# Performance work log

Measured on AMD Instinct MI355X. Metric: run time of the kernel, lower is better.

Reference implementation:

```python
import jax, jax.numpy as jnp
import numpy as np

DIM = 96; HEADS = 3; HEAD_DIM = 32; INNER = HEADS * HEAD_DIM; MLP = 384
WS = 4; WV = WS ** 3; SHIFT = WS // 2  # displacement = window//2
SPATIAL = 64


def _rel_indices():
    c = np.stack(np.meshgrid(np.arange(WS), np.arange(WS), np.arange(WS), indexing='ij'), -1).reshape(-1, 3)
    return c[:, None] - c[None, :] + (WS - 1)  # [WV, WV, 3] in [0, 2*WS-2]

REL = _rel_indices()


def _make_mask():
    # standard Swin shifted-window mask: label contiguity regions, partition, -inf cross-region
    X = Y = Z = SPATIAL
    lab = np.zeros((X, Y, Z), np.int32); cnt = 0
    sl = (slice(0, -WS), slice(-WS, -SHIFT), slice(-SHIFT, None))
    for sx in sl:
        for sy in sl:
            for sz in sl:
                lab[sx, sy, sz] = cnt; cnt += 1
    n = X // WS
    lab = lab.reshape(n, WS, n, WS, n, WS).transpose(0, 2, 4, 1, 3, 5).reshape(-1, WV)
    m = np.where(lab[:, :, None] != lab[:, None, :], -1e9, 0.0).astype(np.float32)
    return jnp.asarray(m)  # [nW, WV, WV]

MASK = _make_mask()


def _ln(x, g, b):
    m = x.mean(-1, keepdims=True)
    v = ((x - m) ** 2).mean(-1, keepdims=True)
    return (x - m) * jax.lax.rsqrt(v + 1e-5) * g + b


def _window_attn(x, W_qkv, W_out, b_out, pos_tab):
    B, X, Y, Z, _ = x.shape
    x = jnp.roll(x, (-SHIFT, -SHIFT, -SHIFT), axis=(1, 2, 3))  # cyclic shift
    qkv = x @ W_qkv  # [B,X,Y,Z,3*INNER]
    nx, ny, nz = X // WS, Y // WS, Z // WS
    qkv = qkv.reshape(B, nx, WS, ny, WS, nz, WS, 3, HEADS, HEAD_DIM)
    qkv = qkv.transpose(7, 0, 8, 1, 3, 5, 2, 4, 6, 9).reshape(3, B, HEADS, nx * ny * nz, WV, HEAD_DIM)
    q, k, v = qkv[0], qkv[1], qkv[2]
    dots = jnp.einsum('bhwid,bhwjd->bhwij', q, k) * (HEAD_DIM ** -0.5)
    bias = pos_tab[REL[..., 0], REL[..., 1], REL[..., 2]]  # [WV,WV]
    dots = dots + bias + MASK[None, None]
    attn = jax.nn.softmax(dots, axis=-1)
    out = jnp.einsum('bhwij,bhwjd->bhwid', attn, v)
    out = out.reshape(B, HEADS, nx, ny, nz, WS, WS, WS, HEAD_DIM)
    out = out.transpose(0, 2, 5, 3, 6, 4, 7, 1, 8).reshape(B, X, Y, Z, INNER)
    out = out @ W_out + b_out
    return jnp.roll(out, (SHIFT, SHIFT, SHIFT), axis=(1, 2, 3))  # cyclic back-shift


def setup_inputs() -> dict:
    key = jax.random.key(0)
    ks = jax.random.split(key, 8)
    w = lambda k, shape, s=0.02: (jax.random.normal(k, shape, jnp.float32) * s)
    return {
        'x': jax.random.normal(ks[0], (1, SPATIAL, SPATIAL, SPATIAL, DIM), jnp.float32),
        'W_qkv': w(ks[1], (DIM, 3 * INNER)),
        'W_out': w(ks[2], (INNER, DIM)),
        'b_out': jnp.zeros((DIM,), jnp.float32),
        'pos_tab': w(ks[3], (2 * WS - 1, 2 * WS - 1, 2 * WS - 1), 1.0),
        'ln1_g': jnp.ones((DIM,), jnp.float32), 'ln1_b': jnp.zeros((DIM,), jnp.float32),
        'ln2_g': jnp.ones((DIM,), jnp.float32), 'ln2_b': jnp.zeros((DIM,), jnp.float32),
        'W1': w(ks[4], (DIM, MLP)), 'b1': jnp.zeros((MLP,), jnp.float32),
        'W2': w(ks[5], (MLP, DIM)), 'b2': jnp.zeros((DIM,), jnp.float32),
    }


def reference(x, W_qkv, W_out, b_out, pos_tab, ln1_g, ln1_b, ln2_g, ln2_b, W1, b1, W2, b2):
    # Residual(PreNorm(WindowAttention3D))
    x = x + _window_attn(_ln(x, ln1_g, ln1_b), W_qkv, W_out, b_out, pos_tab)
    # Residual(PreNorm(FeedForward3D)): Linear -> GELU -> Linear (dropout=0)
    h = _ln(x, ln2_g, ln2_b)
    h = jax.nn.gelu(h @ W1 + b1, approximate=False) @ W2 + b2
    return x + h
```

## Files before the change

### kernel.cpp

```cpp
#include <hip/hip_runtime.h>
#include <hip/hip_bf16.h>

typedef __attribute__((ext_vector_type(8))) short bf16x8;
typedef __attribute__((ext_vector_type(4))) short s16x4;
typedef __attribute__((ext_vector_type(4))) float f32x4;

#define NWIN 4096

__device__ __forceinline__ unsigned short f2bf(float f) {
    __hip_bfloat16 h = __float2bfloat16(f);
    unsigned short u;
    __builtin_memcpy(&u, &h, 2);
    return u;
}
__device__ __forceinline__ float bf2f(unsigned short u) {
    return __uint_as_float(((unsigned int)u) << 16);
}
__device__ __forceinline__ int region(int g) { return (g >= 60) + (g >= 62); }

__global__ void convert_weights(const float* __restrict__ Wqkv, const float* __restrict__ Wout,
                                const float* __restrict__ W1, const float* __restrict__ W2,
                                unsigned short* __restrict__ wq_t, unsigned short* __restrict__ wo_t,
                                unsigned short* __restrict__ w1_t, unsigned short* __restrict__ w2_t) {
    int idx = blockIdx.x * blockDim.x + threadIdx.x;
    if (idx < 27648) {
        int n = idx / 96, k = idx % 96;
        wq_t[idx] = f2bf(Wqkv[k * 288 + n]);
    } else if (idx < 27648 + 9216) {
        int i = idx - 27648; int n = i / 96, k = i % 96;
        wo_t[i] = f2bf(Wout[k * 96 + n]);
    } else if (idx < 27648 + 9216 + 36864) {
        int i = idx - 36864; int n = i / 96, k = i % 96;
        w1_t[i] = f2bf(W1[k * 384 + n]);
    } else if (idx < 110592) {
        int i = idx - 73728; int n = i / 384, k = i % 384;
        w2_t[i] = f2bf(W2[k * 96 + n]);
    }
}

__global__ __launch_bounds__(384, 4) void ln_qkv_attn_kernel(
    const float* __restrict__ x,
    const float* __restrict__ ln1_g, const float* __restrict__ ln1_b,
    const unsigned short* __restrict__ wq_t,
    const float* __restrict__ pos_tab,
    unsigned short* __restrict__ a_out)
{
    __shared__ __align__(16) unsigned short SH[22272];
    __shared__ __align__(16) float posl[344];
    unsigned short* q_s = SH;
    unsigned short* k_s = SH + 7680;
    unsigned short* vT  = SH + 15360;
    unsigned short* y_s = SH + 15360;
    unsigned short* P_s = SH;

    int win = blockIdx.x;
    int tid = threadIdx.x;
    int w = tid >> 6, lane = tid & 63, lr = lane & 15, kh = lane >> 4;
    int ix = win >> 8, iy = (win >> 4) & 15, iz = win & 15;

    if (tid < 343) posl[tid] = pos_tab[tid];

    {
        int grp = tid >> 4, gi = tid & 15;
        float gv[6], bv[6];
        #pragma unroll
        for (int j = 0; j < 6; ++j) { gv[j] = ln1_g[gi + 16 * j]; bv[j] = ln1_b[gi + 16 * j]; }
        #pragma unroll
        for (int p = 0; p < 3; ++p) {
            int t = grp + p * 24;
            if (t < 64) {
                int wx = t >> 4, wy = (t >> 2) & 3, wz = t & 3;
                int sx = (ix * 4 + wx + 2) & 63, sy = (iy * 4 + wy + 2) & 63, sz = (iz * 4 + wz + 2) & 63;
                const float* src = x + ((size_t)((sx * 64 + sy) * 64 + sz)) * 96;
                float v[6]; float s = 0.f, sq = 0.f;
                #pragma unroll
                for (int j = 0; j < 6; ++j) { v[j] = src[gi + 16 * j]; s += v[j]; sq += v[j] * v[j]; }
                #pragma unroll
                for (int m = 8; m >= 1; m >>= 1) { s += __shfl_xor(s, m, 16); sq += __shfl_xor(sq, m, 16); }
                float mean = s * (1.0f / 96.0f);
                float var = sq * (1.0f / 96.0f) - mean * mean;
                float rstd = rsqrtf(var + 1e-5f);
                #pragma unroll
                for (int j = 0; j < 6; ++j)
                    y_s[t * 104 + gi + 16 * j] = f2bf((v[j] - mean) * rstd * gv[j] + bv[j]);
            }
        }
    }
    __syncthreads();

    f32x4 acc3[4][3];
    {
        #pragma unroll
        for (int m = 0; m < 4; ++m)
            #pragma unroll
            for (int n = 0; n < 3; ++n) acc3[m][n] = (f32x4){0.f, 0.f, 0.f, 0.f};
        #pragma unroll
        for (int ks = 0; ks < 3; ++ks) {
            int k0 = ks * 32;
            bf16x8 a[4], bb[3];
            #pragma unroll
            for (int m = 0; m < 4; ++m)
                a[m] = *(const bf16x8*)&y_s[(m * 16 + lr) * 104 + k0 + kh * 8];
            #pragma unroll
            for (int n = 0; n < 3; ++n)
                bb[n] = *(const bf16x8*)(wq_t + (size_t)(w * 48 + n * 16 + lr) * 96 + k0 + kh * 8);
            #pragma unroll
            for (int m = 0; m < 4; ++m)
                #pragma unroll
                for (int n = 0; n < 3; ++n)
                    acc3[m][n] = __builtin_amdgcn_mfma_f32_16x16x32_bf16(a[m], bb[n], acc3[m][n], 0, 0, 0);
        }
    }
    __syncthreads();

    {
        const float scale = 0.17677669529663689f;
        #pragma unroll
        for (int n = 0; n < 3; ++n) {
            int base = w * 48 + n * 16;
            int qq = base / 96, cc0 = base % 96;
            int hh = cc0 >> 5, d0 = cc0 & 31;
            if (qq == 2) {
                #pragma unroll
                for (int m = 0; m < 4; ++m) {
                    s16x4 pv;
                    #pragma unroll
                    for (int r = 0; r < 4; ++r) pv[r] = (short)f2bf(acc3[m][n][r]);
                    *(s16x4*)&vT[(hh * 32 + d0 + lr) * 72 + m * 16 + kh * 4] = pv;
                }
            } else {
                unsigned short* dst = (qq == 0) ? q_s : k_s;
                float sc = (qq == 0) ? scale : 1.0f;
                #pragma unroll
                for (int m = 0; m < 4; ++m)
                    #pragma unroll
                    for (int r = 0; r < 4; ++r) {
                        int tok = m * 16 + kh * 4 + r;
                        dst[(hh * 64 + tok) * 40 + d0 + lr] = f2bf(acc3[m][n][r] * sc);
                    }
            }
        }
    }
    __syncthreads();

    int h3 = w >> 1, rb = (w & 1) * 32;
    f32x4 sa[2][4];
    {
        bf16x8 aq[2], bk[4];
        #pragma unroll
        for (int mm = 0; mm < 2; ++mm)
            aq[mm] = *(const bf16x8*)&q_s[(h3 * 64 + rb + mm * 16 + lr) * 40 + kh * 8];
        #pragma unroll
        for (int n = 0; n < 4; ++n)
            bk[n] = *(const bf16x8*)&k_s[(h3 * 64 + n * 16 + lr) * 40 + kh * 8];
        #pragma unroll
        for (int mm = 0; mm < 2; ++mm)
            #pragma unroll
            for (int n = 0; n < 4; ++n)
                sa[mm][n] = __builtin_amdgcn_mfma_f32_16x16x32_bf16(aq[mm], bk[n], (f32x4){0.f,0.f,0.f,0.f}, 0, 0, 0);

        int labj[4], jwx[4], jwy[4], jwz[4];
        #pragma unroll
        for (int n = 0; n < 4; ++n) {
            int j = n * 16 + lr;
            jwx[n] = j >> 4; jwy[n] = (j >> 2) & 3; jwz[n] = j & 3;
            labj[n] = 9 * region(ix * 4 + jwx[n]) + 3 * region(iy * 4 + jwy[n]) + region(iz * 4 + jwz[n]);
        }
        #pragma unroll
        for (int mm = 0; mm < 2; ++mm)
            #pragma unroll
            for (int r = 0; r < 4; ++r) {
                int i = rb + mm * 16 + kh * 4 + r;
                int iwx = i >> 4, iwy = (i >> 2) & 3, iwz = i & 3;
                int labi = 9 * region(ix * 4 + iwx) + 3 * region(iy * 4 + iwy) + region(iz * 4 + iwz);
                #pragma unroll
                for (int n = 0; n < 4; ++n) {
                    float bias = posl[((iwx - jwx[n] + 3) * 7 + (iwy - jwy[n] + 3)) * 7 + (iwz - jwz[n] + 3)];
                    sa[mm][n][r] += bias + (labi != labj[n] ? -1e9f : 0.0f);
                }
                float mx = fmaxf(fmaxf(sa[mm][0][r], sa[mm][1][r]), fmaxf(sa[mm][2][r], sa[mm][3][r]));
                #pragma unroll
                for (int s = 1; s < 16; s <<= 1) mx = fmaxf(mx, __shfl_xor(mx, s, 16));
                float e0 = __expf(sa[mm][0][r] - mx), e1 = __expf(sa[mm][1][r] - mx);
                float e2 = __expf(sa[mm][2][r] - mx), e3 = __expf(sa[mm][3][r] - mx);
                float sum = e0 + e1 + e2 + e3;
                #pragma unroll
                for (int s = 1; s < 16; s <<= 1) sum += __shfl_xor(sum, s, 16);
                float rs = 1.0f / sum;
                sa[mm][0][r] = e0 * rs; sa[mm][1][r] = e1 * rs;
                sa[mm][2][r] = e2 * rs; sa[mm][3][r] = e3 * rs;
            }
    }
    __syncthreads();

    #pragma unroll
    for (int mm = 0; mm < 2; ++mm)
        #pragma unroll
        for (int n = 0; n < 4; ++n)
            #pragma unroll
            for (int r = 0; r < 4; ++r)
                P_s[(h3 * 64 + rb + mm * 16 + kh * 4 + r) * 72 + n * 16 + lr] = f2bf(sa[mm][n][r]);
    __syncthreads();

    {
        f32x4 oa[2][2];
        #pragma unroll
        for (int mm = 0; mm < 2; ++mm)
            #pragma unroll
            for (int n = 0; n < 2; ++n) oa[mm][n] = (f32x4){0.f, 0.f, 0.f, 0.f};
        #pragma unroll
        for (int ks = 0; ks < 2; ++ks) {
            int k0 = ks * 32;
            bf16x8 ap[2], bv[2];
            #pragma unroll
            for (int mm = 0; mm < 2; ++mm)
                ap[mm] = *(const bf16x8*)&P_s[(h3 * 64 + rb + mm * 16 + lr) * 72 + k0 + kh * 8];
            #pragma unroll
            for (int n = 0; n < 2; ++n)
                bv[n] = *(const bf16x8*)&vT[(h3 * 32 + n * 16 + lr) * 72 + k0 + kh * 8];
            #pragma unroll
            for (int mm = 0; mm < 2; ++mm)
                #pragma unroll
                for (int n = 0; n < 2; ++n)
                    oa[mm][n] = __builtin_amdgcn_mfma_f32_16x16x32_bf16(ap[mm], bv[n], oa[mm][n], 0, 0, 0);
        }
        #pragma unroll
        for (int mm = 0; mm < 2; ++mm)
            #pragma unroll
            for (int n = 0; n < 2; ++n)
                #pragma unroll
                for (int r = 0; r < 4; ++r) {
                    int tok = rb + mm * 16 + kh * 4 + r;
                    a_out[((size_t)win * 64 + tok) * 96 + h3 * 32 + n * 16 + lr] = f2bf(oa[mm][n][r]);
                }
    }
}

__global__ __launch_bounds__(256, 4) void proj_mlp5_kernel(
    const unsigned short* __restrict__ a_out,
    const unsigned short* __restrict__ wo_t, const float* __restrict__ b_out,
    const float* __restrict__ x,
    const float* __restrict__ g2, const float* __restrict__ bt2,
    const unsigned short* __restrict__ w1_t, const float* __restrict__ b1,
    const unsigned short* __restrict__ w2_t, const float* __restrict__ b2,
    float* __restrict__ out)
{
    __shared__ __align__(16) unsigned short SH[13312];
    unsigned short* xl = SH;
    unsigned short* gl = SH + 6656;
    float* tile = (float*)SH;

    int win = blockIdx.x;
    int tid = threadIdx.x;
    int w = tid >> 6, lane = tid & 63, lr = lane & 15, kh = lane >> 4;
    int ix = win >> 8, iy = (win >> 4) & 15, iz = win & 15;
    int tb = w * 16;

    int px = (ix * 4 + w + 2) & 63;
    int py = (iy * 4 + kh + 2) & 63;
    int rowbase = (px * 64 + py) * 64;
    int o[4];
    #pragma unroll
    for (int r = 0; r < 4; ++r) o[r] = (rowbase + ((iz * 4 + r + 2) & 63)) * 96;

    float x1v[6][4];
    {
        f32x4 pa[6];
        #pragma unroll
        for (int n = 0; n < 6; ++n) pa[n] = (f32x4){0.f, 0.f, 0.f, 0.f};
        #pragma unroll
        for (int ks = 0; ks < 3; ++ks) {
            int k0 = ks * 32;
            bf16x8 a = *(const bf16x8*)(a_out + ((size_t)win * 64 + tb + lr) * 96 + k0 + kh * 8);
            #pragma unroll
            for (int n = 0; n < 6; ++n) {
                bf16x8 bb = *(const bf16x8*)(wo_t + (size_t)(n * 16 + lr) * 96 + k0 + kh * 8);
                pa[n] = __builtin_amdgcn_mfma_f32_16x16x32_bf16(a, bb, pa[n], 0, 0, 0);
            }
        }
        #pragma unroll
        for (int n = 0; n < 6; ++n) {
            int c = n * 16 + lr;
            float bo = b_out[c];
            #pragma unroll
            for (int r = 0; r < 4; ++r)
                x1v[n][r] = x[o[r] + c] + pa[n][r] + bo;
        }
        float g2c[6], bc2[6];
        #pragma unroll
        for (int n = 0; n < 6; ++n) { g2c[n] = g2[n * 16 + lr]; bc2[n] = bt2[n * 16 + lr]; }
        #pragma unroll
        for (int r = 0; r < 4; ++r) {
            float s = 0.f, sq = 0.f;
            #pragma unroll
            for (int n = 0; n < 6; ++n) { s += x1v[n][r]; sq += x1v[n][r] * x1v[n][r]; }
            #pragma unroll
            for (int m = 8; m >= 1; m >>= 1) { s += __shfl_xor(s, m, 16); sq += __shfl_xor(sq, m, 16); }
            float mean = s * (1.0f / 96.0f);
            float var = sq * (1.0f / 96.0f) - mean * mean;
            float rstd = rsqrtf(var + 1e-5f);
            int t = tb + kh * 4 + r;
            #pragma unroll
            for (int n = 0; n < 6; ++n)
                xl[t * 104 + n * 16 + lr] = f2bf((x1v[n][r] - mean) * rstd * g2c[n] + bc2[n]);
        }
    }
    __syncthreads();

    int wm = w & 1, wn = w >> 1;
    f32x4 acc2[2][3];
    #pragma unroll
    for (int mf = 0; mf < 2; ++mf)
        #pragma unroll
        for (int nf = 0; nf < 3; ++nf) acc2[mf][nf] = (f32x4){0.f, 0.f, 0.f, 0.f};

    for (int ch = 0; ch < 4; ++ch) {
        f32x4 a1[2][3];
        #pragma unroll
        for (int mf = 0; mf < 2; ++mf)
            #pragma unroll
            for (int nf = 0; nf < 3; ++nf) a1[mf][nf] = (f32x4){0.f, 0.f, 0.f, 0.f};
        #pragma unroll
        for (int ks = 0; ks < 3; ++ks) {
            int k0 = ks * 32;
            bf16x8 af[2], bfr[3];
            #pragma unroll
            for (int mf = 0; mf < 2; ++mf)
                af[mf] = *(const bf16x8*)&xl[(wm * 32 + mf * 16 + lr) * 104 + k0 + kh * 8];
            #pragma unroll
            for (int nf = 0; nf < 3; ++nf)
                bfr[nf] = *(const bf16x8*)(w1_t + (size_t)(ch * 96 + wn * 48 + nf * 16 + lr) * 96 + k0 + kh * 8);
            #pragma unroll
            for (int mf = 0; mf < 2; ++mf)
                #pragma unroll
                for (int nf = 0; nf < 3; ++nf)
                    a1[mf][nf] = __builtin_amdgcn_mfma_f32_16x16x32_bf16(af[mf], bfr[nf], a1[mf][nf], 0, 0, 0);
        }
        #pragma unroll
        for (int nf = 0; nf < 3; ++nf) {
            int lcol = wn * 48 + nf * 16 + lr;
            float bias = b1[ch * 96 + lcol];
            #pragma unroll
            for (int mf = 0; mf < 2; ++mf)
                #pragma unroll
                for (int r = 0; r < 4; ++r) {
                    float u = a1[mf][nf][r] + bias;
                    float t = 1.5957691216057308f * (u + 0.044715f * u * u * u);
                    float ge = u * __builtin_amdgcn_rcpf(1.0f + __expf(-t));
                    gl[(wm * 32 + mf * 16 + kh * 4 + r) * 104 + lcol] = f2bf(ge);
                }
        }
        __syncthreads();
        #pragma unroll
        for (int kc = 0; kc < 3; ++kc) {
            int k0 = kc * 32;
            bf16x8 ag[2];
            #pragma unroll
            for (int mf = 0; mf < 2; ++mf)
                ag[mf] = *(const bf16x8*)&gl[(wm * 32 + mf * 16 + lr) * 104 + k0 + kh * 8];
            #pragma unroll
            for (int nf = 0; nf < 3; ++nf) {
                bf16x8 bb = *(const bf16x8*)(w2_t + (size_t)(wn * 48 + nf * 16 + lr) * 384 + ch * 96 + k0 + kh * 8);
                #pragma unroll
                for (int mf = 0; mf < 2; ++mf)
                    acc2[mf][nf] = __builtin_amdgcn_mfma_f32_16x16x32_bf16(ag[mf], bb, acc2[mf][nf], 0, 0, 0);
            }
        }
        __syncthreads();
    }

    #pragma unroll
    for (int r = 0; r < 4; ++r) {
        int t = tb + kh * 4 + r;
        #pragma unroll
        for (int n = 0; n < 6; ++n)
            tile[t * 100 + n * 16 + lr] = x1v[n][r];
    }
    __syncthreads();
    #pragma unroll
    for (int nf = 0; nf < 3; ++nf) {
        int col = wn * 48 + nf * 16 + lr;
        float bc = b2[col];
        #pragma unroll
        for (int mf = 0; mf < 2; ++mf)
            #pragma unroll
            for (int r = 0; r < 4; ++r) {
                int row = wm * 32 + mf * 16 + kh * 4 + r;
                tile[row * 100 + col] += acc2[mf][nf][r] + bc;
            }
    }
    __syncthreads();
    {
        int token = tid / 24;
        int c4 = tid - token * 24;
        #pragma unroll
        for (int j = 0; j < 6; ++j) {
            int wx = token >> 4, wy = (token >> 2) & 3, wz = token & 3;
            int qx = (ix * 4 + wx + 2) & 63, qy = (iy * 4 + wy + 2) & 63, qz = (iz * 4 + wz + 2) & 63;
            size_t g = ((size_t)((qx * 64 + qy) * 64 + qz)) * 96 + c4 * 4;
            f32x4 v = *(const f32x4*)&tile[token * 100 + c4 * 4];
            *(f32x4*)&out[g] = v;
            token += 10; c4 += 16;
            if (c4 >= 24) { c4 -= 24; token += 1; }
        }
    }
}

extern "C" void kernel_launch(void* const* d_in, const int* in_sizes, int n_in,
                              void* d_out, int out_size, void* d_ws, size_t ws_size,
                              hipStream_t stream) {
    const float* x       = (const float*)d_in[0];
    const float* Wqkv    = (const float*)d_in[1];
    const float* Wout    = (const float*)d_in[2];
    const float* b_out   = (const float*)d_in[3];
    const float* pos_tab = (const float*)d_in[4];
    const float* ln1_g   = (const float*)d_in[5];
    const float* ln1_b   = (const float*)d_in[6];
    const float* ln2_g   = (const float*)d_in[7];
    const float* ln2_b   = (const float*)d_in[8];
    const float* W1      = (const float*)d_in[9];
    const float* b1      = (const float*)d_in[10];
    const float* W2      = (const float*)d_in[11];
    const float* b2      = (const float*)d_in[12];
    float* out = (float*)d_out;

    char* ws = (char*)d_ws;
    unsigned short* a_out = (unsigned short*)(ws);
    unsigned short* wq_t  = (unsigned short*)(ws + 50331648);
    unsigned short* wo_t  = wq_t + 27648;
    unsigned short* w1_t  = wo_t + 9216;
    unsigned short* w2_t  = w1_t + 36864;

    convert_weights<<<432, 256, 0, stream>>>(Wqkv, Wout, W1, W2, wq_t, wo_t, w1_t, w2_t);
    ln_qkv_attn_kernel<<<NWIN, 384, 0, stream>>>(x, ln1_g, ln1_b, wq_t, pos_tab, a_out);
    proj_mlp5_kernel<<<NWIN, 256, 0, stream>>>(a_out, wo_t, b_out, x,
                                               ln2_g, ln2_b, w1_t, b1, w2_t, b2, out);
}
```

Measured before the change: 231.9 us.

## Double-buffer GELU tile to overlap MLP first and second GEMM chunks

The MLP loop now keeps two LDS buffers for the GELU activations. Each iteration computes the next chunk's first GEMM while it runs the second GEMM on the current chunk, which cuts the barriers per chunk from two to one. The residual x loads are also issued before the output-projection MFMAs to hide their latency. In exchange, LDS use grows by half, register pressure rises, and occupancy could drop.

```diff
diff --git a/kernel.cpp b/kernel.cpp
--- a/kernel.cpp
+++ b/kernel.cpp
@@ -236,7 +236,7 @@
     }
 }
 
-__global__ __launch_bounds__(256, 4) void proj_mlp5_kernel(
+__global__ __launch_bounds__(256, 4) void proj_mlp9_kernel(
     const unsigned short* __restrict__ a_out,
     const unsigned short* __restrict__ wo_t, const float* __restrict__ b_out,
     const float* __restrict__ x,
@@ -245,9 +245,8 @@
     const unsigned short* __restrict__ w2_t, const float* __restrict__ b2,
     float* __restrict__ out)
 {
-    __shared__ __align__(16) unsigned short SH[13312];
+    __shared__ __align__(16) unsigned short SH[19968];
     unsigned short* xl = SH;
-    unsigned short* gl = SH + 6656;
     float* tile = (float*)SH;
 
     int win = blockIdx.x;
@@ -265,6 +264,14 @@
 
     float x1v[6][4];
     {
+        #pragma unroll
+        for (int n = 0; n < 6; ++n) {
+            int c = n * 16 + lr;
+            float bo = b_out[c];
+            #pragma unroll
+            for (int r = 0; r < 4; ++r)
+                x1v[n][r] = x[o[r] + c] + bo;
+        }
         f32x4 pa[6];
         #pragma unroll
         for (int n = 0; n < 6; ++n) pa[n] = (f32x4){0.f, 0.f, 0.f, 0.f};
@@ -279,13 +286,10 @@
             }
         }
         #pragma unroll
-        for (int n = 0; n < 6; ++n) {
-            int c = n * 16 + lr;
-            float bo = b_out[c];
+        for (int n = 0; n < 6; ++n)
             #pragma unroll
             for (int r = 0; r < 4; ++r)
-                x1v[n][r] = x[o[r] + c] + pa[n][r] + bo;
-        }
+                x1v[n][r] += pa[n][r];
         float g2c[6], bc2[6];
         #pragma unroll
         for (int n = 0; n < 6; ++n) { g2c[n] = g2[n * 16 + lr]; bc2[n] = bt2[n * 16 + lr]; }
@@ -314,8 +318,7 @@
         #pragma unroll
         for (int nf = 0; nf < 3; ++nf) acc2[mf][nf] = (f32x4){0.f, 0.f, 0.f, 0.f};
 
-    for (int ch = 0; ch < 4; ++ch) {
-        f32x4 a1[2][3];
+    auto G1 = [&](int ch, f32x4 (&a1)[2][3]) {
         #pragma unroll
         for (int mf = 0; mf < 2; ++mf)
             #pragma unroll
@@ -336,6 +339,9 @@
                 for (int nf = 0; nf < 3; ++nf)
                     a1[mf][nf] = __builtin_amdgcn_mfma_f32_16x16x32_bf16(af[mf], bfr[nf], a1[mf][nf], 0, 0, 0);
         }
+    };
+    auto GST = [&](int ch, f32x4 (&a1)[2][3]) {
+        unsigned short* glb = SH + 6656 + (ch & 1) * 6656;
         #pragma unroll
         for (int nf = 0; nf < 3; ++nf) {
             int lcol = wn * 48 + nf * 16 + lr;
@@ -347,17 +353,19 @@
                     float u = a1[mf][nf][r] + bias;
                     float t = 1.5957691216057308f * (u + 0.044715f * u * u * u);
                     float ge = u * __builtin_amdgcn_rcpf(1.0f + __expf(-t));
-                    gl[(wm * 32 + mf * 16 + kh * 4 + r) * 104 + lcol] = f2bf(ge);
+                    glb[(wm * 32 + mf * 16 + kh * 4 + r) * 104 + lcol] = f2bf(ge);
                 }
         }
-        __syncthreads();
+    };
+    auto G2 = [&](int ch) {
+        const unsigned short* glb = SH + 6656 + (ch & 1) * 6656;
         #pragma unroll
         for (int kc = 0; kc < 3; ++kc) {
             int k0 = kc * 32;
             bf16x8 ag[2];
             #pragma unroll
             for (int mf = 0; mf < 2; ++mf)
-                ag[mf] = *(const bf16x8*)&gl[(wm * 32 + mf * 16 + lr) * 104 + k0 + kh * 8];
+                ag[mf] = *(const bf16x8*)&glb[(wm * 32 + mf * 16 + lr) * 104 + k0 + kh * 8];
             #pragma unroll
             for (int nf = 0; nf < 3; ++nf) {
                 bf16x8 bb = *(const bf16x8*)(w2_t + (size_t)(wn * 48 + nf * 16 + lr) * 384 + ch * 96 + k0 + kh * 8);
@@ -366,7 +374,19 @@
                     acc2[mf][nf] = __builtin_amdgcn_mfma_f32_16x16x32_bf16(ag[mf], bb, acc2[mf][nf], 0, 0, 0);
             }
         }
+    };
+
+    {
+        f32x4 a1[2][3];
+        G1(0, a1); GST(0, a1);
         __syncthreads();
+        for (int ch = 0; ch < 4; ++ch) {
+            f32x4 nx[2][3];
+            if (ch < 3) G1(ch + 1, nx);
+            G2(ch);
+            if (ch < 3) GST(ch + 1, nx);
+            __syncthreads();
+        }
     }
 
     #pragma unroll
@@ -433,6 +453,6 @@
 
     convert_weights<<<432, 256, 0, stream>>>(Wqkv, Wout, W1, W2, wq_t, wo_t, w1_t, w2_t);
     ln_qkv_attn_kernel<<<NWIN, 384, 0, stream>>>(x, ln1_g, ln1_b, wq_t, pos_tab, a_out);
-    proj_mlp5_kernel<<<NWIN, 256, 0, stream>>>(a_out, wo_t, b_out, x,
+    proj_mlp9_kernel<<<NWIN, 256, 0, stream>>>(a_out, wo_t, b_out, x,
                                                ln2_g, ln2_b, w1_t, b1, w2_t, b2, out);
 }
```

Result: no change. 233.0 us (+0.5%).
